# Performance work log

Measured on AMD Instinct MI355X. Metric: run time of the kernel, lower is better.

## Reference

```python
import jax, jax.numpy as jnp
import numpy as np

N_TOKENS = 16384
HIDDEN = 1024
FFN = 4 * HIDDEN
N_EXPERTS = 8
TOP_K = 2


def setup_inputs() -> dict:
    key = jax.random.key(0)
    ks = jax.random.split(key, 7)
    s = 0.02
    return {
        "x": jax.random.normal(ks[0], (N_TOKENS, HIDDEN), jnp.float32),
        "Wg": jax.random.normal(ks[1], (HIDDEN, N_EXPERTS), jnp.float32) * s,
        "bg": jnp.zeros((N_EXPERTS,), jnp.float32),
        "W1": jax.random.normal(ks[2], (N_EXPERTS, HIDDEN, FFN), jnp.float32) * s,
        "b1": jnp.zeros((N_EXPERTS, FFN), jnp.float32),
        "W2": jax.random.normal(ks[3], (N_EXPERTS, FFN, HIDDEN), jnp.float32) * s,
        "b2": jnp.zeros((N_EXPERTS, HIDDEN), jnp.float32),
    }


def reference(x, Wg, bg, W1, b1, W2, b2):
    # Gate + top-k routing (softmax over the k selected logits, as in the torch code)
    gate_scores = x @ Wg + bg                              # [N, E]
    topk_scores, topk_idx = jax.lax.top_k(gate_scores, TOP_K)  # [N, k]
    topk_w = jax.nn.softmax(topk_scores, axis=1)           # [N, k]

    n, e = gate_scores.shape
    # Dense per-(token, expert) combine weights; zero for non-selected experts.
    w_dense = jnp.zeros((n, e), x.dtype).at[
        jnp.arange(n)[:, None], topk_idx
    ].add(topk_w)                                          # [N, E]

    # Loop over the small fixed expert set; tokens fully vectorized per expert.
    out = jnp.zeros_like(x)
    for ei in range(e):
        h = jax.nn.relu(x @ W1[ei] + b1[ei])               # [N, FFN]
        y = h @ W2[ei] + b2[ei]                            # [N, H]
        out = out + y * w_dense[:, ei:ei + 1]
    return out
```

## Files before the change

kernel.cpp:

```cpp
#include <hip/hip_runtime.h>
#include <stdint.h>

#define N_TOKENS 16384
#define HIDDEN   1024
#define FFN      4096
#define N_EXPERTS 8
#define NBLK     (N_TOKENS / 256)
#define MAX_T    136
#define MAX_ROWS (MAX_T * 256)
#define NB_HALF  2048

typedef __attribute__((ext_vector_type(8))) short short8;
typedef __attribute__((ext_vector_type(4))) float f32x4;

__device__ inline unsigned short f2bf(float f) {
  union { float f; unsigned u; } c; c.f = f;
  unsigned u = c.u;
  unsigned r = (u + 0x7fffu + ((u >> 16) & 1u)) >> 16;
  return (unsigned short)r;
}

__device__ inline void gld_lds16(const unsigned short* g, unsigned short* l) {
  __builtin_amdgcn_global_load_lds(
      (const __attribute__((address_space(1))) void*)g,
      (__attribute__((address_space(3))) void*)l, 16, 0, 0);
}

#define VM_BAR(N) asm volatile("s_waitcnt vmcnt(" #N ")\n\ts_barrier" ::: "memory")
#define JUST_BAR() asm volatile("s_barrier" ::: "memory")
#define LGKM0()   asm volatile("s_waitcnt lgkmcnt(0)" ::: "memory")
#define PRIO1 __builtin_amdgcn_s_setprio(1)
#define PRIO0 __builtin_amdgcn_s_setprio(0)

__global__ __launch_bounds__(256) void gate_kernel(
    const float* __restrict__ x, const float* __restrict__ Wg,
    const float* __restrict__ bg, int* __restrict__ gate_idx,
    float* __restrict__ gate_w)
{
  int lane = threadIdx.x & 63;
  int wv = threadIdx.x >> 6;
  int t = blockIdx.x * 4 + wv;
  const float* xr = x + (size_t)t * HIDDEN;
  float acc[N_EXPERTS];
#pragma unroll
  for (int e = 0; e < N_EXPERTS; e++) acc[e] = 0.f;
#pragma unroll
  for (int i = 0; i < HIDDEN / 64; i++) {
    int h = i * 64 + lane;
    float xv = xr[h];
    const float4* wv4 = (const float4*)(Wg + (size_t)h * N_EXPERTS);
    float4 w01 = wv4[0], w23 = wv4[1];
    acc[0] = fmaf(xv, w01.x, acc[0]); acc[1] = fmaf(xv, w01.y, acc[1]);
    acc[2] = fmaf(xv, w01.z, acc[2]); acc[3] = fmaf(xv, w01.w, acc[3]);
    acc[4] = fmaf(xv, w23.x, acc[4]); acc[5] = fmaf(xv, w23.y, acc[5]);
    acc[6] = fmaf(xv, w23.z, acc[6]); acc[7] = fmaf(xv, w23.w, acc[7]);
  }
#pragma unroll
  for (int off = 32; off > 0; off >>= 1)
#pragma unroll
    for (int e = 0; e < N_EXPERTS; e++)
      acc[e] += __shfl_down(acc[e], off, 64);
  if (lane == 0) {
    float s[N_EXPERTS];
#pragma unroll
    for (int e = 0; e < N_EXPERTS; e++) s[e] = acc[e] + bg[e];
    int e0 = 0;
#pragma unroll
    for (int e = 1; e < N_EXPERTS; e++) if (s[e] > s[e0]) e0 = e;
    int e1 = (e0 == 0) ? 1 : 0;
#pragma unroll
    for (int e = 0; e < N_EXPERTS; e++) if (e != e0 && s[e] > s[e1]) e1 = e;
    float d = s[e1] - s[e0];
    float ex = __expf(d);
    float w0 = 1.f / (1.f + ex);
    float w1 = ex / (1.f + ex);
    gate_idx[2 * t] = e0; gate_idx[2 * t + 1] = e1;
    gate_w[2 * t] = w0;  gate_w[2 * t + 1] = w1;
  }
}

__global__ __launch_bounds__(256) void count_kernel(
    const int* __restrict__ gate_idx, int* __restrict__ blockCounts)
{
  __shared__ int h[N_EXPERTS];
  if (threadIdx.x < N_EXPERTS) h[threadIdx.x] = 0;
  __syncthreads();
  int t = blockIdx.x * 256 + threadIdx.x;
  atomicAdd(&h[gate_idx[2 * t]], 1);
  atomicAdd(&h[gate_idx[2 * t + 1]], 1);
  __syncthreads();
  if (threadIdx.x < N_EXPERTS)
    blockCounts[blockIdx.x * N_EXPERTS + threadIdx.x] = h[threadIdx.x];
}

__global__ void scan_kernel(const int* __restrict__ blockCounts,
                            int* __restrict__ blockBase, int* __restrict__ meta)
{
  __shared__ int totals[N_EXPERTS];
  __shared__ int offs[N_EXPERTS + 1];
  int e = threadIdx.x;
  if (e < N_EXPERTS) {
    int run = 0;
    for (int b = 0; b < NBLK; b++) {
      blockBase[b * N_EXPERTS + e] = run;
      run += blockCounts[b * N_EXPERTS + e];
    }
    totals[e] = run;
  }
  __syncthreads();
  if (threadIdx.x == 0) {
    int off = 0;
    for (int ee = 0; ee < N_EXPERTS; ee++) {
      offs[ee] = off;
      meta[16 + ee] = off;
      off += ((totals[ee] + 255) >> 8) << 8;
    }
    offs[N_EXPERTS] = off;
    meta[16 + N_EXPERTS] = off;
    int ntiles = off >> 8;
    meta[25] = ntiles;
    int ee = 0;
    for (int t = 0; t < ntiles; t++) {
      while (offs[ee + 1] <= (t << 8)) ee++;
      meta[32 + t] = ee;
    }
  }
  __syncthreads();
  if (e < N_EXPERTS) {
    int o = offs[e];
    for (int b = 0; b < NBLK; b++)
      blockBase[b * N_EXPERTS + e] += o;
  }
}

__global__ __launch_bounds__(256) void place_kernel(
    const int* __restrict__ gate_idx, const float* __restrict__ gate_w,
    const int* __restrict__ blockBase, int* __restrict__ pair_token,
    float* __restrict__ pair_w)
{
  __shared__ int cur[N_EXPERTS];
  if (threadIdx.x < N_EXPERTS)
    cur[threadIdx.x] = blockBase[blockIdx.x * N_EXPERTS + threadIdx.x];
  __syncthreads();
  int t = blockIdx.x * 256 + threadIdx.x;
#pragma unroll
  for (int k = 0; k < 2; k++) {
    int e = gate_idx[2 * t + k];
    int pos = atomicAdd(&cur[e], 1);
    pair_token[pos] = t;
    pair_w[pos] = gate_w[2 * t + k];
  }
}

__global__ __launch_bounds__(256) void gather_kernel(
    const float* __restrict__ x, const int* __restrict__ pair_token,
    unsigned short* __restrict__ Xg)
{
  int r = blockIdx.x;
  int t = pair_token[r];
  if (t < 0) return;
  const float4* src = (const float4*)(x + (size_t)t * HIDDEN);
  float4 v = src[threadIdx.x];
  ushort4 o;
  o.x = f2bf(v.x); o.y = f2bf(v.y); o.z = f2bf(v.z); o.w = f2bf(v.w);
  ((ushort4*)(Xg + (size_t)r * HIDDEN))[threadIdx.x] = o;
}

__global__ __launch_bounds__(256) void transpose_bf16_kernel(
    const float* __restrict__ in, unsigned short* __restrict__ out, int R, int C)
{
  __shared__ float tile[64][65];
  int e = blockIdx.z;
  int r0 = blockIdx.y * 64, c0 = blockIdx.x * 64;
  int tr = threadIdx.x >> 4, tc = threadIdx.x & 15;
  const float* src = in + ((size_t)e * R + r0) * C + c0;
#pragma unroll
  for (int rr = 0; rr < 4; rr++) {
    int row = rr * 16 + tr;
    float4 v = *(const float4*)(src + (size_t)row * C + tc * 4);
    tile[row][tc * 4 + 0] = v.x; tile[row][tc * 4 + 1] = v.y;
    tile[row][tc * 4 + 2] = v.z; tile[row][tc * 4 + 3] = v.w;
  }
  __syncthreads();
  unsigned short* dst = out + ((size_t)e * C + c0) * R + r0;
#pragma unroll
  for (int rr = 0; rr < 4; rr++) {
    int crow = rr * 16 + tr;
    ushort4 o;
    o.x = f2bf(tile[tc * 4 + 0][crow]);
    o.y = f2bf(tile[tc * 4 + 1][crow]);
    o.z = f2bf(tile[tc * 4 + 2][crow]);
    o.w = f2bf(tile[tc * 4 + 3][crow]);
    *(ushort4*)(dst + (size_t)crow * R + tc * 4) = o;
  }
}

template<int EPI>
__global__ __launch_bounds__(512, 2) void moe_gemm_kernel(
    const unsigned short* __restrict__ A,
    const unsigned short* __restrict__ Bt,
    const float* __restrict__ bias,
    unsigned short* __restrict__ Hout,
    float* __restrict__ out,
    const int* __restrict__ meta,
    const int* __restrict__ pair_token,
    const float* __restrict__ pair_w,
    int lda, int ldb, int bkoff, int klen, int nbase, int nbfull)
{
  int ntiles = meta[25];

  int gx = gridDim.x;
  int nwg = gx * gridDim.y;
  int lid = blockIdx.y * gx + blockIdx.x;
  int q = nwg >> 3, r8 = nwg & 7;
  int xcd = lid & 7, pos = lid >> 3;
  int aid = (xcd < r8 ? xcd * (q + 1) : r8 * (q + 1) + (xcd - r8) * q) + pos;
  int rt = aid / gx;
  int ct = aid % gx;
  if (rt >= ntiles) return;
  int row0 = rt << 8;
  int e = meta[32 + rt];

  __shared__ __align__(16) unsigned short lds[2][4][8192];

  int tid = threadIdx.x;
  int lane = tid & 63, wv = tid >> 6;
  int wm = wv >> 2, wn = wv & 3;
  int quad = lane >> 4, l16 = lane & 15;

  int r0c = tid >> 3;
  int c0c = (tid & 7) ^ (r0c & 7);
  const unsigned short* Ab = A + (size_t)row0 * lda;
  const unsigned short* Bb = Bt + ((size_t)e * nbfull + nbase + (ct << 8)) * ldb + bkoff;
  const unsigned short* gA0 = Ab + (size_t)r0c * lda + c0c * 8;
  const unsigned short* gB0 = Bb + (size_t)r0c * ldb + c0c * 8;
  size_t sA = (size_t)64 * lda, sB = (size_t)64 * ldb;

  auto STAGE = [&](int bi, int slot, const unsigned short* g, size_t s64, int k0) {
    unsigned short* l = &lds[bi][slot][0] + tid * 8;
    gld_lds16(g + k0, l);
    gld_lds16(g + s64 + k0, l + 4096);
  };

  int swz0 = (quad ^ (l16 & 7)) << 3;
  int swz1 = ((quad ^ 4) ^ (l16 & 7)) << 3;
  int aoff0 = wm * 1024 + l16 * 64 + swz0;
  int aoff1 = wm * 1024 + l16 * 64 + swz1;
  int boff0 = wn * 1024 + l16 * 64 + swz0;
  int boff1 = wn * 1024 + l16 * 64 + swz1;

  f32x4 acc[8][4];
  f32x4 zero = {0.f, 0.f, 0.f, 0.f};
#pragma unroll
  for (int i = 0; i < 8; i++)
#pragma unroll
    for (int j = 0; j < 4; j++) acc[i][j] = zero;

  short8 aL[4][2], aH[4][2], bL[2][2], bH[2][2];

  auto LDA = [&](int bi, int half, short8 (&d)[4][2]) {
    const unsigned short* base = &lds[bi][half][0];
#pragma unroll
    for (int mf = 0; mf < 4; mf++) {
      d[mf][0] = *(const short8*)(base + aoff0 + mf * 2048);
      d[mf][1] = *(const short8*)(base + aoff1 + mf * 2048);
    }
  };
  auto LDB = [&](int bi, int half, short8 (&d)[2][2]) {
    const unsigned short* base = &lds[bi][2 + half][0];
#pragma unroll
    for (int nf = 0; nf < 2; nf++) {
      d[nf][0] = *(const short8*)(base + boff0 + nf * 4096);
      d[nf][1] = *(const short8*)(base + boff1 + nf * 4096);
    }
  };
  auto MM = [&](short8 (&a)[4][2], short8 (&b)[2][2], int mh, int nh) {
#pragma unroll
    for (int mf = 0; mf < 4; mf++)
#pragma unroll
      for (int nf = 0; nf < 2; nf++) {
        f32x4& c = acc[mh * 4 + mf][nh * 2 + nf];
        c = __builtin_amdgcn_mfma_f32_16x16x32_bf16(a[mf][0], b[nf][0], c, 0, 0, 0);
        c = __builtin_amdgcn_mfma_f32_16x16x32_bf16(a[mf][1], b[nf][1], c, 0, 0, 0);
      }
  };

  int NT = klen >> 6;

  STAGE(0, 0, gA0, sA, 0);
  STAGE(0, 2, gB0, sB, 0);
  STAGE(0, 1, gA0 + 2 * sA, sA, 0);
  STAGE(0, 3, gB0 + 2 * sB, sB, 0);
  VM_BAR(4);

  for (int t = 0; t < NT - 1; t++) {
    int bi = t & 1, nb = bi ^ 1;
    int kn = (t + 1) << 6;
    LDA(bi, 0, aL); LDB(bi, 0, bL);
    STAGE(nb, 0, gA0, sA, kn);
    VM_BAR(4);
    LGKM0();
    PRIO1; MM(aL, bL, 0, 0); PRIO0;
    JUST_BAR();
    LDA(bi, 1, aH);
    STAGE(nb, 2, gB0, sB, kn);
    VM_BAR(4);
    LGKM0();
    PRIO1; MM(aH, bL, 1, 0); PRIO0;
    JUST_BAR();
    LDB(bi, 1, bH);
    STAGE(nb, 1, gA0 + 2 * sA, sA, kn);
    VM_BAR(4);
    LGKM0();
    PRIO1; MM(aL, bH, 0, 1); PRIO0;
    JUST_BAR();
    STAGE(nb, 3, gB0 + 2 * sB, sB, kn);
    VM_BAR(4);
    PRIO1; MM(aH, bH, 1, 1); PRIO0;
    JUST_BAR();
  }
  {
    int bi = (NT - 1) & 1;
    LDA(bi, 0, aL); LDB(bi, 0, bL);
    VM_BAR(2);
    LGKM0();
    PRIO1; MM(aL, bL, 0, 0); PRIO0;
    JUST_BAR();
    LDA(bi, 1, aH);
    VM_BAR(0);
    LGKM0();
    PRIO1; MM(aH, bL, 1, 0); PRIO0;
    JUST_BAR();
    LDB(bi, 1, bH);
    LGKM0();
    PRIO1; MM(aL, bH, 0, 1); PRIO0;
    PRIO1; MM(aH, bH, 1, 1); PRIO0;
  }

  if (EPI == 0) {
#pragma unroll
    for (int mi = 0; mi < 8; mi++) {
      size_t hr = (size_t)row0 + (mi * 2 + wm) * 16 + quad * 4;
#pragma unroll
      for (int ni = 0; ni < 4; ni++) {
        int hcol = (ct << 8) + (ni * 4 + wn) * 16 + l16;
        float bb = bias[(size_t)e * nbfull + nbase + hcol];
#pragma unroll
        for (int j = 0; j < 4; j++) {
          float v = fmaxf(acc[mi][ni][j] + bb, 0.f);
          Hout[(hr + j) * (size_t)NB_HALF + hcol] = f2bf(v);
        }
      }
    }
  } else {
#pragma unroll
    for (int mi = 0; mi < 8; mi++) {
      int rbase = row0 + (mi * 2 + wm) * 16 + quad * 4;
      int tok[4]; float wgt[4];
#pragma unroll
      for (int j = 0; j < 4; j++) {
        tok[j] = pair_token[rbase + j];
        wgt[j] = pair_w[rbase + j];
      }
#pragma unroll
      for (int ni = 0; ni < 4; ni++) {
        int gcol = (ct << 8) + (ni * 4 + wn) * 16 + l16;
        float bb = bias ? bias[(size_t)e * nbfull + gcol] : 0.f;
#pragma unroll
        for (int j = 0; j < 4; j++) {
          if (tok[j] >= 0)
            atomicAdd(out + (size_t)tok[j] * HIDDEN + gcol,
                      wgt[j] * (acc[mi][ni][j] + bb));
        }
      }
    }
  }
}

extern "C" void kernel_launch(void* const* d_in, const int* in_sizes, int n_in,
                              void* d_out, int out_size, void* d_ws, size_t ws_size,
                              hipStream_t stream)
{
  const float* x  = (const float*)d_in[0];
  const float* Wg = (const float*)d_in[1];
  const float* bg = (const float*)d_in[2];
  const float* W1 = (const float*)d_in[3];
  const float* b1 = (const float*)d_in[4];
  const float* W2 = (const float*)d_in[5];
  const float* b2 = (const float*)d_in[6];
  float* out = (float*)d_out;

  char* ws = (char*)d_ws;
  size_t off = 0;
  auto alloc = [&](size_t bytes) {
    char* p = ws + off;
    off += (bytes + 255) & ~(size_t)255;
    return p;
  };
  int* gate_idx          = (int*)alloc((size_t)N_TOKENS * 2 * sizeof(int));
  float* gate_w          = (float*)alloc((size_t)N_TOKENS * 2 * sizeof(float));
  int* meta              = (int*)alloc(2048);
  int* blockCounts       = (int*)alloc((size_t)NBLK * N_EXPERTS * sizeof(int));
  int* blockBase         = (int*)alloc((size_t)NBLK * N_EXPERTS * sizeof(int));
  int* pair_token        = (int*)alloc((size_t)MAX_ROWS * sizeof(int));
  float* pair_w          = (float*)alloc((size_t)MAX_ROWS * sizeof(float));
  unsigned short* Xg     = (unsigned short*)alloc((size_t)MAX_ROWS * HIDDEN * 2);
  unsigned short* W1T    = (unsigned short*)alloc((size_t)N_EXPERTS * FFN * HIDDEN * 2);
  unsigned short* W2T    = (unsigned short*)alloc((size_t)N_EXPERTS * HIDDEN * FFN * 2);
  unsigned short* H      = (unsigned short*)alloc((size_t)MAX_ROWS * NB_HALF * 2);

  hipMemsetAsync(pair_token, 0xFF, (size_t)MAX_ROWS * sizeof(int), stream);
  hipMemsetAsync(out, 0, (size_t)N_TOKENS * HIDDEN * sizeof(float), stream);

  gate_kernel<<<N_TOKENS / 4, 256, 0, stream>>>(x, Wg, bg, gate_idx, gate_w);
  count_kernel<<<NBLK, 256, 0, stream>>>(gate_idx, blockCounts);
  scan_kernel<<<1, 64, 0, stream>>>(blockCounts, blockBase, meta);
  place_kernel<<<NBLK, 256, 0, stream>>>(gate_idx, gate_w, blockBase,
                                         pair_token, pair_w);
  gather_kernel<<<MAX_ROWS, 256, 0, stream>>>(x, pair_token, Xg);
  transpose_bf16_kernel<<<dim3(FFN / 64, HIDDEN / 64, N_EXPERTS), 256, 0, stream>>>(
      W1, W1T, HIDDEN, FFN);
  transpose_bf16_kernel<<<dim3(HIDDEN / 64, FFN / 64, N_EXPERTS), 256, 0, stream>>>(
      W2, W2T, FFN, HIDDEN);

  for (int fh = 0; fh < 2; fh++) {
    int nb = fh * NB_HALF;
    moe_gemm_kernel<0><<<dim3(NB_HALF / 256, MAX_T), 512, 0, stream>>>(
        Xg, W1T, b1, H, nullptr, meta, nullptr, nullptr,
        HIDDEN, HIDDEN, 0, HIDDEN, nb, FFN);
    moe_gemm_kernel<1><<<dim3(HIDDEN / 256, MAX_T), 512, 0, stream>>>(
        H, W2T, fh == 0 ? b2 : nullptr, nullptr, out, meta, pair_token, pair_w,
        NB_HALF, FFN, nb, NB_HALF, 0, HIDDEN);
  }
}
```

Baseline: 1.397 ms.

## Deepen GEMM k-loop prefetch to keep three stages of loads in flight

Restructures the double-buffered GEMM main loop so global-to-LDS staging runs further ahead. Three quarter-tiles of the next k-step are prefetched before the loop, and inside the loop the remaining quarter for k+1 and three quarters for k+2 are issued while the current tile is multiplied. VM waits are relaxed to allow six outstanding loads, and the MFMA quarter order is changed so buffer regions are freed before they are overwritten. The goal is to hide more global-memory latency behind MFMA work. In exchange, the LDS buffer reuse ordering becomes tricky, and a wrong wait count could race.

```diff
diff --git a/kernel.cpp b/kernel.cpp
--- a/kernel.cpp
+++ b/kernel.cpp
@@ -291,50 +291,69 @@
   STAGE(0, 2, gB0, sB, 0);
   STAGE(0, 1, gA0 + 2 * sA, sA, 0);
   STAGE(0, 3, gB0 + 2 * sB, sB, 0);
-  VM_BAR(4);
-
-  for (int t = 0; t < NT - 1; t++) {
+  STAGE(1, 0, gA0, sA, 64);
+  STAGE(1, 2, gB0, sB, 64);
+  STAGE(1, 1, gA0 + 2 * sA, sA, 64);
+  VM_BAR(6);
+
+  for (int t = 0; t <= NT - 3; t++) {
     int bi = t & 1, nb = bi ^ 1;
-    int kn = (t + 1) << 6;
+    int kc = (t + 1) << 6, kn = (t + 2) << 6;
     LDA(bi, 0, aL); LDB(bi, 0, bL);
-    STAGE(nb, 0, gA0, sA, kn);
+    STAGE(nb, 3, gB0 + 2 * sB, sB, kc);
+    JUST_BAR();
+    LGKM0();
+    PRIO1; MM(aL, bL, 0, 0); PRIO0;
+    JUST_BAR();
+    LDB(bi, 1, bH);
+    STAGE(bi, 0, gA0, sA, kn);
+    JUST_BAR();
+    LGKM0();
+    PRIO1; MM(aL, bH, 0, 1); PRIO0;
+    JUST_BAR();
+    LDA(bi, 1, aH);
+    STAGE(bi, 2, gB0, sB, kn);
+    JUST_BAR();
+    LGKM0();
+    PRIO1; MM(aH, bL, 1, 0); PRIO0;
+    JUST_BAR();
+    STAGE(bi, 1, gA0 + 2 * sA, sA, kn);
+    VM_BAR(6);
+    PRIO1; MM(aH, bH, 1, 1); PRIO0;
+    JUST_BAR();
+  }
+  {
+    int bi = (NT - 2) & 1, nb = bi ^ 1;
+    int kc = (NT - 1) << 6;
+    LDA(bi, 0, aL); LDB(bi, 0, bL);
+    STAGE(nb, 3, gB0 + 2 * sB, sB, kc);
+    VM_BAR(6);
+    LGKM0();
+    PRIO1; MM(aL, bL, 0, 0); PRIO0;
+    JUST_BAR();
+    LDB(bi, 1, bH);
     VM_BAR(4);
     LGKM0();
-    PRIO1; MM(aL, bL, 0, 0); PRIO0;
+    PRIO1; MM(aL, bH, 0, 1); PRIO0;
     JUST_BAR();
     LDA(bi, 1, aH);
-    STAGE(nb, 2, gB0, sB, kn);
-    VM_BAR(4);
+    VM_BAR(2);
     LGKM0();
     PRIO1; MM(aH, bL, 1, 0); PRIO0;
     JUST_BAR();
-    LDB(bi, 1, bH);
-    STAGE(nb, 1, gA0 + 2 * sA, sA, kn);
-    VM_BAR(4);
-    LGKM0();
-    PRIO1; MM(aL, bH, 0, 1); PRIO0;
-    JUST_BAR();
-    STAGE(nb, 3, gB0 + 2 * sB, sB, kn);
-    VM_BAR(4);
+    VM_BAR(0);
     PRIO1; MM(aH, bH, 1, 1); PRIO0;
     JUST_BAR();
   }
   {
     int bi = (NT - 1) & 1;
     LDA(bi, 0, aL); LDB(bi, 0, bL);
-    VM_BAR(2);
-    LGKM0();
-    PRIO1; MM(aL, bL, 0, 0); PRIO0;
-    JUST_BAR();
-    LDA(bi, 1, aH);
-    VM_BAR(0);
-    LGKM0();
-    PRIO1; MM(aH, bL, 1, 0); PRIO0;
-    JUST_BAR();
-    LDB(bi, 1, bH);
-    LGKM0();
-    PRIO1; MM(aL, bH, 0, 1); PRIO0;
-    PRIO1; MM(aH, bH, 1, 1); PRIO0;
+    LDB(bi, 1, bH); LDA(bi, 1, aH);
+    LGKM0();
+    PRIO1;
+    MM(aL, bL, 0, 0); MM(aL, bH, 0, 1);
+    MM(aH, bL, 1, 0); MM(aH, bH, 1, 1);
+    PRIO0;
   }
 
   if (EPI == 0) {
```

After: 1.392 ms. About the same (-0.3%).

## Replace direct global-to-LDS loads with register-staged prefetch and one barrier per tile

Applied to the files above, without the earlier changes.

Replaces the global_load_lds direct-to-LDS staging, which used four sub-stage barriers per k-tile, with a register-staged scheme. Each k-tile's next A/B tiles are loaded into registers up front, all MFMAs for the current tile run, and then the registers are written swizzled into the alternate LDS buffer, followed by a single barrier. This cuts the barrier count and the fine-grained vmcnt waits. In exchange it adds VGPR pressure for the 8 staging vectors and extra ds_write instructions, and the hand-tuned interleave is replaced by sched_barrier fences.

```diff
diff --git a/kernel.cpp b/kernel.cpp
--- a/kernel.cpp
+++ b/kernel.cpp
@@ -20,15 +20,11 @@
   return (unsigned short)r;
 }
 
-__device__ inline void gld_lds16(const unsigned short* g, unsigned short* l) {
-  __builtin_amdgcn_global_load_lds(
-      (const __attribute__((address_space(1))) void*)g,
-      (__attribute__((address_space(3))) void*)l, 16, 0, 0);
-}
-
-#define VM_BAR(N) asm volatile("s_waitcnt vmcnt(" #N ")\n\ts_barrier" ::: "memory")
-#define JUST_BAR() asm volatile("s_barrier" ::: "memory")
-#define LGKM0()   asm volatile("s_waitcnt lgkmcnt(0)" ::: "memory")
+#define SCHED0() __builtin_amdgcn_sched_barrier(0)
+static __device__ __forceinline__ void BAR() {
+  SCHED0(); __builtin_amdgcn_s_barrier(); SCHED0();
+}
+#define LGKM0() do { SCHED0(); asm volatile("s_waitcnt lgkmcnt(0)"); SCHED0(); } while (0)
 #define PRIO1 __builtin_amdgcn_s_setprio(1)
 #define PRIO0 __builtin_amdgcn_s_setprio(0)
 
@@ -232,14 +228,31 @@
   int c0c = (tid & 7) ^ (r0c & 7);
   const unsigned short* Ab = A + (size_t)row0 * lda;
   const unsigned short* Bb = Bt + ((size_t)e * nbfull + nbase + (ct << 8)) * ldb + bkoff;
-  const unsigned short* gA0 = Ab + (size_t)r0c * lda + c0c * 8;
-  const unsigned short* gB0 = Bb + (size_t)r0c * ldb + c0c * 8;
+  const unsigned short* gA0 = Ab + (size_t)r0c * lda + (tid & 7) * 8;
+  const unsigned short* gB0 = Bb + (size_t)r0c * ldb + (tid & 7) * 8;
   size_t sA = (size_t)64 * lda, sB = (size_t)64 * ldb;
 
-  auto STAGE = [&](int bi, int slot, const unsigned short* g, size_t s64, int k0) {
-    unsigned short* l = &lds[bi][slot][0] + tid * 8;
-    gld_lds16(g + k0, l);
-    gld_lds16(g + s64 + k0, l + 4096);
+  f32x4 st[8];
+  auto LOADS = [&](int k0) {
+    st[0] = *(const f32x4*)(gA0 + k0);
+    st[1] = *(const f32x4*)(gA0 + sA + k0);
+    st[2] = *(const f32x4*)(gA0 + 2 * sA + k0);
+    st[3] = *(const f32x4*)(gA0 + 3 * sA + k0);
+    st[4] = *(const f32x4*)(gB0 + k0);
+    st[5] = *(const f32x4*)(gB0 + sB + k0);
+    st[6] = *(const f32x4*)(gB0 + 2 * sB + k0);
+    st[7] = *(const f32x4*)(gB0 + 3 * sB + k0);
+  };
+  auto WRITES = [&](int nb) {
+    unsigned short* p = &lds[nb][0][0] + ((size_t)r0c * 8 + c0c) * 8;
+    *(f32x4*)(p)         = st[0];
+    *(f32x4*)(p + 4096)  = st[1];
+    *(f32x4*)(p + 8192)  = st[2];
+    *(f32x4*)(p + 12288) = st[3];
+    *(f32x4*)(p + 16384) = st[4];
+    *(f32x4*)(p + 20480) = st[5];
+    *(f32x4*)(p + 24576) = st[6];
+    *(f32x4*)(p + 28672) = st[7];
   };
 
   int swz0 = (quad ^ (l16 & 7)) << 3;
@@ -256,8 +269,6 @@
 #pragma unroll
     for (int j = 0; j < 4; j++) acc[i][j] = zero;
 
-  short8 aL[4][2], aH[4][2], bL[2][2], bH[2][2];
-
   auto LDA = [&](int bi, int half, short8 (&d)[4][2]) {
     const unsigned short* base = &lds[bi][half][0];
 #pragma unroll
@@ -287,54 +298,27 @@
 
   int NT = klen >> 6;
 
-  STAGE(0, 0, gA0, sA, 0);
-  STAGE(0, 2, gB0, sB, 0);
-  STAGE(0, 1, gA0 + 2 * sA, sA, 0);
-  STAGE(0, 3, gB0 + 2 * sB, sB, 0);
-  VM_BAR(4);
-
-  for (int t = 0; t < NT - 1; t++) {
+  LOADS(0);
+  WRITES(0);
+  LGKM0();
+  BAR();
+
+  for (int t = 0; t < NT; t++) {
     int bi = t & 1, nb = bi ^ 1;
-    int kn = (t + 1) << 6;
+    bool pf = (t + 1 < NT);
+    if (pf) LOADS((t + 1) << 6);
+    SCHED0();
+    short8 aL[4][2], aH[4][2], bL[2][2], bH[2][2];
     LDA(bi, 0, aL); LDB(bi, 0, bL);
-    STAGE(nb, 0, gA0, sA, kn);
-    VM_BAR(4);
+    PRIO1; MM(aL, bL, 0, 0); PRIO0;
+    LDB(bi, 1, bH);
+    PRIO1; MM(aL, bH, 0, 1); PRIO0;
+    LDA(bi, 1, aH);
+    PRIO1; MM(aH, bL, 1, 0); MM(aH, bH, 1, 1); PRIO0;
+    SCHED0();
+    if (pf) WRITES(nb);
     LGKM0();
-    PRIO1; MM(aL, bL, 0, 0); PRIO0;
-    JUST_BAR();
-    LDA(bi, 1, aH);
-    STAGE(nb, 2, gB0, sB, kn);
-    VM_BAR(4);
-    LGKM0();
-    PRIO1; MM(aH, bL, 1, 0); PRIO0;
-    JUST_BAR();
-    LDB(bi, 1, bH);
-    STAGE(nb, 1, gA0 + 2 * sA, sA, kn);
-    VM_BAR(4);
-    LGKM0();
-    PRIO1; MM(aL, bH, 0, 1); PRIO0;
-    JUST_BAR();
-    STAGE(nb, 3, gB0 + 2 * sB, sB, kn);
-    VM_BAR(4);
-    PRIO1; MM(aH, bH, 1, 1); PRIO0;
-    JUST_BAR();
-  }
-  {
-    int bi = (NT - 1) & 1;
-    LDA(bi, 0, aL); LDB(bi, 0, bL);
-    VM_BAR(2);
-    LGKM0();
-    PRIO1; MM(aL, bL, 0, 0); PRIO0;
-    JUST_BAR();
-    LDA(bi, 1, aH);
-    VM_BAR(0);
-    LGKM0();
-    PRIO1; MM(aH, bL, 1, 0); PRIO0;
-    JUST_BAR();
-    LDB(bi, 1, bH);
-    LGKM0();
-    PRIO1; MM(aL, bH, 0, 1); PRIO0;
-    PRIO1; MM(aH, bH, 1, 1); PRIO0;
+    BAR();
   }
 
   if (EPI == 0) {
```

Measured after the change: 1.478 ms. 1.06x slower.
